# Optimization experiments

Hardware: AMD Instinct MI355X
Metric: run time of the kernel (lower is better)

The kernel has to match this reference:

```python
import jax, jax.numpy as jnp
import numpy as np

B, M, F_N, D, GS, L = 32, 512, 64, 128, 4, 8  # batch, max atoms, in feats, int_d, graph channels, layers


def setup_inputs() -> dict:
    key = jax.random.key(0)
    ks = jax.random.split(key, 8)
    G = jax.random.uniform(ks[0], (B, GS, M, M), dtype=jnp.float32)      # dense multi-channel adjacency
    x = jax.random.normal(ks[1], (B, M, F_N), dtype=jnp.float32)          # per-atom features
    W0 = jax.random.normal(ks[2], (GS, F_N, D), dtype=jnp.float32) * 0.05 # per-channel Linear, layer 0
    b0 = jax.random.normal(ks[3], (GS, D), dtype=jnp.float32) * 0.05
    Wl = jax.random.normal(ks[4], (L - 1, GS, D, D), dtype=jnp.float32) * 0.05
    bl = jax.random.normal(ks[5], (L - 1, GS, D), dtype=jnp.float32) * 0.05
    Wout = jax.random.normal(ks[6], (D, 1), dtype=jnp.float32) * 0.05
    bout = jax.random.normal(ks[7], (1,), dtype=jnp.float32) * 0.05
    return {"G": G, "x": x, "W0": W0, "b0": b0, "Wl": Wl, "bl": bl, "Wout": Wout, "bout": bout}


def _graph_mat_layer(G, h, W, b):
    # per-channel linear: [B,M,C] x [GS,C,P] -> [B,GS,M,P]
    multi = jnp.einsum('bmc,gcp->bgmp', h, W) + b[None, :, None, :]
    # per-sample, per-channel adjacency matmul: [B,GS,M,M] @ [B,GS,M,P]
    xout = jnp.einsum('bgmn,bgnp->bgmp', G, multi)
    # ReLU then goodmax aggregation over graph channels (dim=1)
    return jnp.max(jax.nn.relu(xout), axis=1)  # [B,M,P]


def reference(G, x, W0, b0, Wl, bl, Wout, bout):
    # layer 0: input width F_N != D, so no residual (shape mismatch)
    h = _graph_mat_layer(G, x, W0, b0)
    # layers 1..L-1: resnet skip (shapes match)
    for i in range(L - 1):
        h = _graph_mat_layer(G, h, Wl[i], bl[i]) + h
    # lin_out on [B,M,D] -> [B,M,1]
    return h @ Wout + bout
```

## Files before the change

kernel.cpp:

```cpp
#include <hip/hip_runtime.h>
#include <stdint.h>


#define B_  32
#define M_  512
#define FN_ 64
#define D_  128
#define GS_ 4
#define L_  8

typedef __attribute__((ext_vector_type(8))) short short8;
typedef __attribute__((ext_vector_type(4))) float f32x4;
typedef unsigned short us;

__device__ __forceinline__ us f2bf(float f) {
  union { float f; unsigned int u; } v; v.f = f;
  return (us)((v.u + 0x7FFFu + ((v.u >> 16) & 1u)) >> 16);
}

__device__ __forceinline__ short8 cvt8(float4 a, float4 b) {
  union { unsigned int u[4]; short8 s; } r;
  asm("v_cvt_pk_bf16_f32 %0, %1, %2" : "=v"(r.u[0]) : "v"(a.x), "v"(a.y));
  asm("v_cvt_pk_bf16_f32 %0, %1, %2" : "=v"(r.u[1]) : "v"(a.z), "v"(a.w));
  asm("v_cvt_pk_bf16_f32 %0, %1, %2" : "=v"(r.u[2]) : "v"(b.x), "v"(b.y));
  asm("v_cvt_pk_bf16_f32 %0, %1, %2" : "=v"(r.u[3]) : "v"(b.z), "v"(b.w));
  return r.s;
}

__device__ __forceinline__ void gl16(const void* g, void* l) {
  __builtin_amdgcn_global_load_lds((const __attribute__((address_space(1))) void*)g,
                                   (__attribute__((address_space(3))) void*)l, 16, 0, 0);
}

__global__ void k_convW(const float* __restrict__ W0, const float* __restrict__ Wl,
                        us* __restrict__ W0T, us* __restrict__ WlT) {
  int i = blockIdx.x * blockDim.x + threadIdx.x;
  const int n0 = GS_ * FN_ * D_;
  if (i < n0) {
    int g = i / (FN_ * D_), r = i % (FN_ * D_), c = r / D_, p = r % D_;
    W0T[((size_t)g * D_ + p) * FN_ + c] = f2bf(W0[i]);
  } else {
    int j = i - n0;
    if (j < 7 * GS_ * D_ * D_) {
      int l = j / (GS_ * D_ * D_), r = j % (GS_ * D_ * D_);
      int g = r / (D_ * D_), r2 = r % (D_ * D_), c = r2 / D_, p = r2 % D_;
      WlT[(((size_t)l * GS_ + g) * D_ + p) * D_ + c] = f2bf(Wl[j]);
    }
  }
}

template<int NKA, int CC>
__device__ __forceinline__ void stageA(const us* __restrict__ Wt,
                                       const float* __restrict__ bias,
                                       us* __restrict__ Mw,
                                       const us* hbL, us (*smS)[24576],
                                       int g, int hf, int lr, int kq,
                                       int srow, int scol, int kk, int b, int mt) {
  f32x4 acc[4][4];
#pragma unroll
  for (int i = 0; i < 4; ++i)
#pragma unroll
    for (int j = 0; j < 4; ++j) acc[i][j] = (f32x4){0.f, 0.f, 0.f, 0.f};

#define STGA(bufi, ks) do { \
    us* bb_ = smS[bufi] + g * 6144; \
    _Pragma("unroll") \
    for (int u_ = 0; u_ < 4; ++u_) { \
      const us* sp_ = Wt + (size_t)g * D_ * CC + (size_t)(hf * 64 + u_ * 16 + srow) * CC \
                      + (ks) * 32 + scol; \
      gl16(sp_, bb_ + 2048 + (hf * 4 + u_) * 512); \
    } \
  } while (0)

  STGA(0, 0);
  STGA(1, 1);
  const int cm = (CC == 64) ? 7 : 15;
#pragma unroll
  for (int ks = 0; ks < NKA; ++ks) {
    if (ks < NKA - 1) asm volatile("s_waitcnt vmcnt(4)" ::: "memory");
    else              asm volatile("s_waitcnt vmcnt(0)" ::: "memory");
    __builtin_amdgcn_sched_barrier(0);
    const us* sb = smS[ks % 3] + g * 6144 + 2048;
    short8 af[4], bf[4];
#pragma unroll
    for (int i = 0; i < 4; ++i)
      af[i] = *(const short8*)&hbL[(i * 16 + lr) * 128 + (((ks * 4 + kq) ^ (lr & cm)) << 3)];
#pragma unroll
    for (int j = 0; j < 4; ++j)
      bf[j] = *(const short8*)&sb[(hf * 64 + j * 16 + lr) * 32 + kk];
    if (ks + 2 < NKA) STGA((ks + 2) % 3, ks + 2);
    asm volatile("s_waitcnt lgkmcnt(0)" ::: "memory");
    __builtin_amdgcn_sched_barrier(0);
#pragma unroll
    for (int i = 0; i < 4; ++i)
#pragma unroll
      for (int j = 0; j < 4; ++j)
        acc[i][j] = __builtin_amdgcn_mfma_f32_16x16x32_bf16(af[i], bf[j], acc[i][j], 0, 0, 0);
  }
#undef STGA

#pragma unroll
  for (int j = 0; j < 4; ++j) {
    const int p = hf * 64 + j * 16 + lr;
    const float bv = bias[g * D_ + p];
    us* op = Mw + ((size_t)(b * GS_ + g) * D_ + p) * M_;
#pragma unroll
    for (int i = 0; i < 4; ++i) {
      const int n0 = mt * 64 + i * 16 + kq * 4;
      f32x4 v = acc[i][j];
      ushort4 o;
      o.x = f2bf(v[0] + bv); o.y = f2bf(v[1] + bv);
      o.z = f2bf(v[2] + bv); o.w = f2bf(v[3] + bv);
      *(ushort4*)(op + n0) = o;
    }
  }
}

__launch_bounds__(512, 1)
__global__ void k_pre(const float* __restrict__ x,
                      const us* __restrict__ W0T, const float* __restrict__ b0,
                      us* __restrict__ Mh0) {
  __shared__ __align__(16) us smS[2][24576];
  __shared__ __align__(16) us hbL[8192];

  const int bid = blockIdx.x;
  const int swz = (bid & 7) * 32 + (bid >> 3);
  const int b = swz >> 3, mt = swz & 7;

  const int t = threadIdx.x;
  const int w = t >> 6, g = w >> 1, hf = w & 1;
  const int lane = t & 63, lr = lane & 15, kq = lane >> 4;
  const int srow = lane >> 2;
  const int scol = ((lane & 3) ^ ((lane >> 3) & 3)) * 8;
  const int kk = (kq ^ ((lr >> 1) & 3)) * 8;

  {
    const int row = t >> 3, c8 = t & 7;
    const float* xs = x + ((size_t)b * M_ + mt * 64 + row) * FN_ + c8 * 8;
    float4 v0 = *(const float4*)xs, v1 = *(const float4*)(xs + 4);
    ushort4 o0, o1;
    o0.x = f2bf(v0.x); o0.y = f2bf(v0.y); o0.z = f2bf(v0.z); o0.w = f2bf(v0.w);
    o1.x = f2bf(v1.x); o1.y = f2bf(v1.y); o1.z = f2bf(v1.z); o1.w = f2bf(v1.w);
    us* dp = hbL + row * 128 + ((c8 ^ (row & 7)) << 3);
    *(ushort4*)dp = o0; *(ushort4*)(dp + 4) = o1;
  }
  __syncthreads();

  stageA<FN_ / 32, FN_>(W0T, b0, Mh0, hbL, smS, g, hf, lr, kq, srow, scol, kk, b, mt);
}

__launch_bounds__(512, 1)
__global__ void k_fusedC(const float* __restrict__ G, const us* __restrict__ Min,
                         us* __restrict__ Mout, us* __restrict__ Gh,
                         const us* __restrict__ WT, const float* __restrict__ bias,
                         float* __restrict__ h) {
  __shared__ __align__(16) us smS[3][24576];
  __shared__ __align__(16) us hbL[8192];

  const int bid = blockIdx.x;
  const int swz = (bid & 7) * 32 + (bid >> 3);
  const int b = swz >> 3, mt = swz & 7;

  const int t = threadIdx.x;
  const int w = t >> 6, g = w >> 1, hf = w & 1;
  const int lane = t & 63, lr = lane & 15, kq = lane >> 4;
  const int srow = lane >> 2;
  const int scol = ((lane & 3) ^ ((lane >> 3) & 3)) * 8;
  const int kk = (kq ^ ((lr >> 1) & 3)) * 8;
  const int m_l = t >> 3, pq = t & 7;

  const float* Ag = G + ((size_t)(b * GS_ + g) * M_ + mt * 64) * M_;
  us* Ghp = Gh + ((size_t)(b * GS_ + g) * M_ + mt * 64) * M_;
  const us* BgB = Min + (size_t)(b * GS_ + g) * D_ * M_;

#define STGC(bufi, ks) do { \
    us* bb_ = smS[bufi] + g * 6144; \
    _Pragma("unroll") \
    for (int u_ = 0; u_ < 4; ++u_) { \
      const int ls_ = 4 + hf * 4 + u_; \
      const us* sp_ = BgB + (size_t)((ls_ - 4) * 16 + srow) * M_ + (ks) * 32 + scol; \
      gl16(sp_, bb_ + ls_ * 512 + lane * 8); \
    } \
  } while (0)

#define LDA(AR, ks) do { \
    _Pragma("unroll") \
    for (int i_ = 0; i_ < 4; ++i_) { \
      const float* ap_ = Ag + (size_t)(i_ * 16 + lr) * M_ + (ks) * 32 + kq * 8; \
      AR[2 * i_]     = *(const float4*)ap_; \
      AR[2 * i_ + 1] = *(const float4*)(ap_ + 4); \
    } \
  } while (0)

#define BODY(ks, AR) do { \
    if ((ks) < 15) asm volatile("s_waitcnt vmcnt(12)" ::: "memory"); \
    else           asm volatile("s_waitcnt vmcnt(0)" ::: "memory"); \
    __builtin_amdgcn_sched_barrier(0); \
    short8 af[4], bf[4]; \
    _Pragma("unroll") \
    for (int i_ = 0; i_ < 4; ++i_) af[i_] = cvt8(AR[2 * i_], AR[2 * i_ + 1]); \
    if (hf == 0) { \
      _Pragma("unroll") \
      for (int i_ = 0; i_ < 4; ++i_) \
        *(short8*)(Ghp + (size_t)(i_ * 16 + lr) * M_ + (ks) * 32 + kq * 8) = af[i_]; \
    } \
    { const us* sb_ = smS[(ks) % 3] + g * 6144 + 2048; \
      _Pragma("unroll") \
      for (int j_ = 0; j_ < 4; ++j_) \
        bf[j_] = *(const short8*)&sb_[(hf * 64 + j_ * 16 + lr) * 32 + kk]; } \
    if ((ks) + 2 < 16) { LDA(AR, (ks) + 2); STGC(((ks) + 2) % 3, (ks) + 2); } \
    asm volatile("s_waitcnt lgkmcnt(0)" ::: "memory"); \
    __builtin_amdgcn_sched_barrier(0); \
    _Pragma("unroll") \
    for (int i_ = 0; i_ < 4; ++i_) \
      _Pragma("unroll") \
      for (int j_ = 0; j_ < 4; ++j_) \
        acc[i_][j_] = __builtin_amdgcn_mfma_f32_16x16x32_bf16(af[i_], bf[j_], acc[i_][j_], 0, 0, 0); \
  } while (0)

  f32x4 acc[4][4];
#pragma unroll
  for (int i = 0; i < 4; ++i)
#pragma unroll
    for (int j = 0; j < 4; ++j) acc[i][j] = (f32x4){0.f, 0.f, 0.f, 0.f};

  float4 aA[8], aB[8];
  LDA(aA, 0); STGC(0, 0);
  LDA(aB, 1); STGC(1, 1);

#pragma unroll
  for (int kp = 0; kp < 8; ++kp) {
    BODY(2 * kp, aA);
    BODY(2 * kp + 1, aB);
  }
#undef BODY
#undef LDA
#undef STGC

  __syncthreads();

  {
    float* red = (float*)smS + (size_t)g * 8192;
#pragma unroll
    for (int i = 0; i < 4; ++i)
#pragma unroll
      for (int j = 0; j < 4; ++j) {
        const int col = hf * 64 + j * 16 + lr;
        const int ch = col >> 2, cw = col & 3;
#pragma unroll
        for (int cc = 0; cc < 4; ++cc) {
          const int row = i * 16 + kq * 4 + cc;
          red[row * 128 + ((ch ^ (row & 7)) << 2) + cw] = fmaxf(acc[i][j][cc], 0.f);
        }
      }
  }
  __syncthreads();

  f32x4 hreg[4];
  {
    const float* red = (const float*)smS;
#pragma unroll
    for (int k = 0; k < 4; ++k) {
      const int ch = pq * 4 + k;
      const float* rp = red + (size_t)m_l * 128 + ((ch ^ (m_l & 7)) << 2);
      f32x4 v = *(const f32x4*)rp;
#pragma unroll
      for (int gg = 1; gg < 4; ++gg) {
        f32x4 u = *(const f32x4*)(rp + (size_t)gg * 8192);
        v[0] = fmaxf(v[0], u[0]); v[1] = fmaxf(v[1], u[1]);
        v[2] = fmaxf(v[2], u[2]); v[3] = fmaxf(v[3], u[3]);
      }
      hreg[k] = v;
    }
  }
  const size_t ho = ((size_t)b * M_ + mt * 64 + m_l) * D_ + pq * 16;
  float4* hp = (float4*)(h + ho);
#pragma unroll
  for (int k = 0; k < 4; ++k)
    hp[k] = (float4){hreg[k][0], hreg[k][1], hreg[k][2], hreg[k][3]};
  us* d0 = hbL + m_l * 128 + (((2 * pq) ^ (m_l & 15)) << 3);
  us* d1 = hbL + m_l * 128 + (((2 * pq + 1) ^ (m_l & 15)) << 3);
  ushort4 o0, o1, o2, o3;
  o0.x = f2bf(hreg[0][0]); o0.y = f2bf(hreg[0][1]); o0.z = f2bf(hreg[0][2]); o0.w = f2bf(hreg[0][3]);
  o1.x = f2bf(hreg[1][0]); o1.y = f2bf(hreg[1][1]); o1.z = f2bf(hreg[1][2]); o1.w = f2bf(hreg[1][3]);
  o2.x = f2bf(hreg[2][0]); o2.y = f2bf(hreg[2][1]); o2.z = f2bf(hreg[2][2]); o2.w = f2bf(hreg[2][3]);
  o3.x = f2bf(hreg[3][0]); o3.y = f2bf(hreg[3][1]); o3.z = f2bf(hreg[3][2]); o3.w = f2bf(hreg[3][3]);
  *(ushort4*)d0 = o0; *(ushort4*)(d0 + 4) = o1;
  *(ushort4*)d1 = o2; *(ushort4*)(d1 + 4) = o3;
  __syncthreads();

  stageA<D_ / 32, D_>(WT, bias, Mout, hbL, (us (*)[24576])smS, g, hf, lr, kq, srow, scol, kk, b, mt);
}

template<int FIRST, int LAST>
__launch_bounds__(512, 1)
__global__ void k_fused(const us* __restrict__ Gh, const us* __restrict__ Min,
                        us* __restrict__ Mout,
                        const us* __restrict__ WT, const float* __restrict__ bias,
                        float* __restrict__ h,
                        const float* __restrict__ Wout, const float* __restrict__ bout,
                        float* __restrict__ out) {
  __shared__ __align__(16) us smS[3][24576];
  __shared__ __align__(16) us hbL[8192];

  const int bid = blockIdx.x;
  const int swz = (bid & 7) * 32 + (bid >> 3);
  const int b = swz >> 3, mt = swz & 7;

  const int t = threadIdx.x;
  const int w = t >> 6, g = w >> 1, hf = w & 1;
  const int lane = t & 63, lr = lane & 15, kq = lane >> 4;
  const int srow = lane >> 2;
  const int scol = ((lane & 3) ^ ((lane >> 3) & 3)) * 8;
  const int kk = (kq ^ ((lr >> 1) & 3)) * 8;
  const int m_l = t >> 3, pq = t & 7;

  const us* AgB = Gh + ((size_t)(b * GS_ + g) * M_ + mt * 64) * M_;
  const us* BgB = Min + (size_t)(b * GS_ + g) * D_ * M_;
  f32x4 acc[4][4];
#pragma unroll
  for (int i = 0; i < 4; ++i)
#pragma unroll
    for (int j = 0; j < 4; ++j) acc[i][j] = (f32x4){0.f, 0.f, 0.f, 0.f};

#define STGB(bufi, ks) do { \
    us* bb_ = smS[bufi] + g * 6144; \
    _Pragma("unroll") \
    for (int u_ = 0; u_ < 6; ++u_) { \
      const int ls_ = hf * 6 + u_; \
      const us* sp_ = (ls_ < 4) \
        ? AgB + (size_t)(ls_ * 16 + srow) * M_ + (ks) * 32 + scol \
        : BgB + (size_t)((ls_ - 4) * 16 + srow) * M_ + (ks) * 32 + scol; \
      gl16(sp_, bb_ + ls_ * 512 + lane * 8); \
    } \
  } while (0)

  STGB(0, 0);
  STGB(1, 1);
#pragma unroll
  for (int ks = 0; ks < 16; ++ks) {
    if (ks < 15) asm volatile("s_waitcnt vmcnt(6)" ::: "memory");
    else         asm volatile("s_waitcnt vmcnt(0)" ::: "memory");
    __builtin_amdgcn_s_barrier();
    __builtin_amdgcn_sched_barrier(0);
    const us* sa = smS[ks % 3] + g * 6144;
    const us* sb = sa + 2048;
    short8 af[4], bf[4];
#pragma unroll
    for (int i = 0; i < 4; ++i)
      af[i] = *(const short8*)&sa[(i * 16 + lr) * 32 + kk];
#pragma unroll
    for (int j = 0; j < 4; ++j)
      bf[j] = *(const short8*)&sb[(hf * 64 + j * 16 + lr) * 32 + kk];
    if (ks + 2 < 16) STGB((ks + 2) % 3, ks + 2);
    asm volatile("s_waitcnt lgkmcnt(0)" ::: "memory");
    __builtin_amdgcn_sched_barrier(0);
#pragma unroll
    for (int i = 0; i < 4; ++i)
#pragma unroll
      for (int j = 0; j < 4; ++j)
        acc[i][j] = __builtin_amdgcn_mfma_f32_16x16x32_bf16(af[i], bf[j], acc[i][j], 0, 0, 0);
  }
#undef STGB

  __builtin_amdgcn_s_barrier();
  __builtin_amdgcn_sched_barrier(0);

  {
    float* red = (float*)smS + (size_t)g * 8192;
#pragma unroll
    for (int i = 0; i < 4; ++i)
#pragma unroll
      for (int j = 0; j < 4; ++j) {
        const int col = hf * 64 + j * 16 + lr;
        const int ch = col >> 2, cw = col & 3;
#pragma unroll
        for (int cc = 0; cc < 4; ++cc) {
          const int row = i * 16 + kq * 4 + cc;
          red[row * 128 + ((ch ^ (row & 7)) << 2) + cw] = fmaxf(acc[i][j][cc], 0.f);
        }
      }
  }
  __builtin_amdgcn_s_barrier();
  __builtin_amdgcn_sched_barrier(0);

  f32x4 hreg[4];
  {
    const float* red = (const float*)smS;
#pragma unroll
    for (int k = 0; k < 4; ++k) {
      const int ch = pq * 4 + k;
      const float* rp = red + (size_t)m_l * 128 + ((ch ^ (m_l & 7)) << 2);
      f32x4 v = *(const f32x4*)rp;
#pragma unroll
      for (int gg = 1; gg < 4; ++gg) {
        f32x4 u = *(const f32x4*)(rp + (size_t)gg * 8192);
        v[0] = fmaxf(v[0], u[0]); v[1] = fmaxf(v[1], u[1]);
        v[2] = fmaxf(v[2], u[2]); v[3] = fmaxf(v[3], u[3]);
      }
      hreg[k] = v;
    }
  }
  const size_t ho = ((size_t)b * M_ + mt * 64 + m_l) * D_ + pq * 16;
  float4* hp = (float4*)(h + ho);
  if (!FIRST) {
#pragma unroll
    for (int k = 0; k < 4; ++k) {
      float4 hv = hp[k];
      hreg[k][0] += hv.x; hreg[k][1] += hv.y; hreg[k][2] += hv.z; hreg[k][3] += hv.w;
    }
  }

  if constexpr (!LAST) {
#pragma unroll
    for (int k = 0; k < 4; ++k)
      hp[k] = (float4){hreg[k][0], hreg[k][1], hreg[k][2], hreg[k][3]};
    us* d0 = hbL + m_l * 128 + (((2 * pq) ^ (m_l & 15)) << 3);
    us* d1 = hbL + m_l * 128 + (((2 * pq + 1) ^ (m_l & 15)) << 3);
    ushort4 o0, o1, o2, o3;
    o0.x = f2bf(hreg[0][0]); o0.y = f2bf(hreg[0][1]); o0.z = f2bf(hreg[0][2]); o0.w = f2bf(hreg[0][3]);
    o1.x = f2bf(hreg[1][0]); o1.y = f2bf(hreg[1][1]); o1.z = f2bf(hreg[1][2]); o1.w = f2bf(hreg[1][3]);
    o2.x = f2bf(hreg[2][0]); o2.y = f2bf(hreg[2][1]); o2.z = f2bf(hreg[2][2]); o2.w = f2bf(hreg[2][3]);
    o3.x = f2bf(hreg[3][0]); o3.y = f2bf(hreg[3][1]); o3.z = f2bf(hreg[3][2]); o3.w = f2bf(hreg[3][3]);
    *(ushort4*)d0 = o0; *(ushort4*)(d0 + 4) = o1;
    *(ushort4*)d1 = o2; *(ushort4*)(d1 + 4) = o3;
    __syncthreads();

    stageA<D_ / 32, D_>(WT, bias, Mout, hbL, smS, g, hf, lr, kq, srow, scol, kk, b, mt);
  } else {
    float s = 0.f;
#pragma unroll
    for (int k = 0; k < 4; ++k) {
      const float4 wv = *(const float4*)(Wout + pq * 16 + k * 4);
      s += hreg[k][0] * wv.x + hreg[k][1] * wv.y + hreg[k][2] * wv.z + hreg[k][3] * wv.w;
    }
    s += __shfl_xor(s, 1);
    s += __shfl_xor(s, 2);
    s += __shfl_xor(s, 4);
    if (pq == 0) out[(size_t)b * M_ + mt * 64 + m_l] = s + bout[0];
  }
}

extern "C" void kernel_launch(void* const* d_in, const int* in_sizes, int n_in,
                              void* d_out, int out_size, void* d_ws, size_t ws_size,
                              hipStream_t stream) {
  const float* G    = (const float*)d_in[0];
  const float* x    = (const float*)d_in[1];
  const float* W0   = (const float*)d_in[2];
  const float* b0   = (const float*)d_in[3];
  const float* Wl   = (const float*)d_in[4];
  const float* bl   = (const float*)d_in[5];
  const float* Wout = (const float*)d_in[6];
  const float* bout = (const float*)d_in[7];

  char* ws = (char*)d_ws;
  us*   Gh  = (us*)(ws);
  us*   Mh0 = (us*)(ws + 67108864);
  us*   Mh1 = (us*)(ws + 83886080);
  float* h  = (float*)(ws + 100663296);
  us*   W0T = (us*)(ws + 109051904);
  us*   WlT = (us*)(ws + 109051904 + 65536);
  float* out = (float*)d_out;

  k_convW<<<1920, 256, 0, stream>>>(W0, Wl, W0T, WlT);
  k_pre<<<256, 512, 0, stream>>>(x, W0T, b0, Mh0);

  k_fusedC<<<256, 512, 0, stream>>>(G, Mh0, Mh1,
      Gh, WlT + (size_t)0 * GS_ * D_ * D_, bl + (size_t)0 * GS_ * D_, h);

  for (int l = 1; l < L_ - 1; ++l) {
    const us* Min = (l & 1) ? Mh1 : Mh0;
    us* Mout      = (l & 1) ? Mh0 : Mh1;
    k_fused<0, 0><<<256, 512, 0, stream>>>(Gh, Min, Mout,
        WlT + (size_t)l * GS_ * D_ * D_, bl + (size_t)l * GS_ * D_,
        h, Wout, bout, out);
  }
  k_fused<0, 1><<<256, 512, 0, stream>>>(Gh, (L_ - 1) & 1 ? Mh1 : Mh0, nullptr,
      nullptr, nullptr, h, Wout, bout, out);
}
```

Before: 274.1 us.

## Stage fp32 adjacency tiles through LDS with double-buffered async loads in first fused layer

The first fused layer kernel previously loaded fp32 G tiles straight into registers and used a triple-buffered LDS ring for only the B operand. It now stages both the fp32 A tile and the bf16 B tile into LDS with async global-to-LDS loads, using a two-stage double buffer and explicit barriers. The bf16 write-back of G is also split across both half-waves instead of being done by one. The intent is to cut register pressure and improve latency hiding for the large fp32 G stream, at the cost of extra LDS traffic and two block barriers per k-step.

```diff
diff --git a/kernel.cpp b/kernel.cpp
--- a/kernel.cpp
+++ b/kernel.cpp
@@ -150,12 +150,12 @@
 }
 
 __launch_bounds__(512, 1)
-__global__ void k_fusedC(const float* __restrict__ G, const us* __restrict__ Min,
-                         us* __restrict__ Mout, us* __restrict__ Gh,
-                         const us* __restrict__ WT, const float* __restrict__ bias,
-                         float* __restrict__ h) {
-  __shared__ __align__(16) us smS[3][24576];
-  __shared__ __align__(16) us hbL[8192];
+__global__ void k_fusedC2(const float* __restrict__ G, const us* __restrict__ Min,
+                          us* __restrict__ Mout, us* __restrict__ Gh,
+                          const us* __restrict__ WT, const float* __restrict__ bias,
+                          float* __restrict__ h) {
+  __shared__ __align__(16) us sm[81920];
+  us* hbL = sm + 73728;
 
   const int bid = blockIdx.x;
   const int swz = (bid & 7) * 32 + (bid >> 3);
@@ -165,82 +165,85 @@
   const int w = t >> 6, g = w >> 1, hf = w & 1;
   const int lane = t & 63, lr = lane & 15, kq = lane >> 4;
   const int srow = lane >> 2;
-  const int scol = ((lane & 3) ^ ((lane >> 3) & 3)) * 8;
+  const int scolB = ((lane & 3) ^ ((lane >> 3) & 3)) * 8;
   const int kk = (kq ^ ((lr >> 1) & 3)) * 8;
+  const int arow = lane >> 3;
+  const int acol = ((lane & 7) ^ (arow & 7)) * 4;
   const int m_l = t >> 3, pq = t & 7;
 
-  const float* Ag = G + ((size_t)(b * GS_ + g) * M_ + mt * 64) * M_;
+  const float* Agf = G + ((size_t)(b * GS_ + g) * M_ + mt * 64) * M_;
   us* Ghp = Gh + ((size_t)(b * GS_ + g) * M_ + mt * 64) * M_;
-  const us* BgB = Min + (size_t)(b * GS_ + g) * D_ * M_;
-
-#define STGC(bufi, ks) do { \
-    us* bb_ = smS[bufi] + g * 6144; \
+  const us* Bg = Min + (size_t)(b * GS_ + g) * D_ * M_;
+
+#define BUF(ks) (((ks) & 1) * 32768 + g * 8192)
+#define STAGE2(ks) do { \
+    us* ab_ = sm + BUF(ks); \
     _Pragma("unroll") \
     for (int u_ = 0; u_ < 4; ++u_) { \
-      const int ls_ = 4 + hf * 4 + u_; \
-      const us* sp_ = BgB + (size_t)((ls_ - 4) * 16 + srow) * M_ + (ks) * 32 + scol; \
-      gl16(sp_, bb_ + ls_ * 512 + lane * 8); \
+      const int s_ = hf * 4 + u_; \
+      gl16(Agf + (size_t)(s_ * 8 + arow) * M_ + (ks) * 32 + acol, \
+           ab_ + s_ * 512 + lane * 8); \
+      gl16(Bg + (size_t)(s_ * 16 + srow) * M_ + (ks) * 32 + scolB, \
+           ab_ + 4096 + s_ * 512 + lane * 8); \
     } \
   } while (0)
 
-#define LDA(AR, ks) do { \
-    _Pragma("unroll") \
-    for (int i_ = 0; i_ < 4; ++i_) { \
-      const float* ap_ = Ag + (size_t)(i_ * 16 + lr) * M_ + (ks) * 32 + kq * 8; \
-      AR[2 * i_]     = *(const float4*)ap_; \
-      AR[2 * i_ + 1] = *(const float4*)(ap_ + 4); \
-    } \
-  } while (0)
-
-#define BODY(ks, AR) do { \
-    if ((ks) < 15) asm volatile("s_waitcnt vmcnt(12)" ::: "memory"); \
-    else           asm volatile("s_waitcnt vmcnt(0)" ::: "memory"); \
-    __builtin_amdgcn_sched_barrier(0); \
-    short8 af[4], bf[4]; \
-    _Pragma("unroll") \
-    for (int i_ = 0; i_ < 4; ++i_) af[i_] = cvt8(AR[2 * i_], AR[2 * i_ + 1]); \
-    if (hf == 0) { \
-      _Pragma("unroll") \
-      for (int i_ = 0; i_ < 4; ++i_) \
-        *(short8*)(Ghp + (size_t)(i_ * 16 + lr) * M_ + (ks) * 32 + kq * 8) = af[i_]; \
-    } \
-    { const us* sb_ = smS[(ks) % 3] + g * 6144 + 2048; \
-      _Pragma("unroll") \
-      for (int j_ = 0; j_ < 4; ++j_) \
-        bf[j_] = *(const short8*)&sb_[(hf * 64 + j_ * 16 + lr) * 32 + kk]; } \
-    if ((ks) + 2 < 16) { LDA(AR, (ks) + 2); STGC(((ks) + 2) % 3, (ks) + 2); } \
-    asm volatile("s_waitcnt lgkmcnt(0)" ::: "memory"); \
-    __builtin_amdgcn_sched_barrier(0); \
-    _Pragma("unroll") \
-    for (int i_ = 0; i_ < 4; ++i_) \
-      _Pragma("unroll") \
-      for (int j_ = 0; j_ < 4; ++j_) \
-        acc[i_][j_] = __builtin_amdgcn_mfma_f32_16x16x32_bf16(af[i_], bf[j_], acc[i_][j_], 0, 0, 0); \
-  } while (0)
-
   f32x4 acc[4][4];
 #pragma unroll
   for (int i = 0; i < 4; ++i)
 #pragma unroll
     for (int j = 0; j < 4; ++j) acc[i][j] = (f32x4){0.f, 0.f, 0.f, 0.f};
 
-  float4 aA[8], aB[8];
-  LDA(aA, 0); STGC(0, 0);
-  LDA(aB, 1); STGC(1, 1);
-
-#pragma unroll
-  for (int kp = 0; kp < 8; ++kp) {
-    BODY(2 * kp, aA);
-    BODY(2 * kp + 1, aB);
-  }
-#undef BODY
-#undef LDA
-#undef STGC
+  STAGE2(0);
+  STAGE2(1);
+
+#pragma unroll
+  for (int ks = 0; ks < 16; ++ks) {
+    if (ks == 0)      asm volatile("s_waitcnt vmcnt(8)" ::: "memory");
+    else if (ks < 15) asm volatile("s_waitcnt vmcnt(10)" ::: "memory");
+    else              asm volatile("s_waitcnt vmcnt(2)" ::: "memory");
+    __builtin_amdgcn_s_barrier();
+    __builtin_amdgcn_sched_barrier(0);
+    const us* ab = sm + BUF(ks);
+    float4 ar[8];
+#pragma unroll
+    for (int i = 0; i < 4; ++i) {
+      const int row = i * 16 + lr;
+#pragma unroll
+      for (int e = 0; e < 2; ++e)
+        ar[2 * i + e] = *(const float4*)&ab[(row * 8 + ((kq * 2 + e) ^ (row & 7))) * 8];
+    }
+    const us* sb = ab + 4096;
+    short8 bf[4];
+#pragma unroll
+    for (int j = 0; j < 4; ++j)
+      bf[j] = *(const short8*)&sb[(hf * 64 + j * 16 + lr) * 32 + kk];
+    asm volatile("s_waitcnt lgkmcnt(0)" ::: "memory");
+    __builtin_amdgcn_sched_barrier(0);
+    short8 af[4];
+#pragma unroll
+    for (int i = 0; i < 4; ++i) af[i] = cvt8(ar[2 * i], ar[2 * i + 1]);
+    __builtin_amdgcn_s_barrier();
+    {
+      const int i0 = hf * 2;
+#pragma unroll
+      for (int ii = 0; ii < 2; ++ii)
+        *(short8*)(Ghp + (size_t)((i0 + ii) * 16 + lr) * M_ + ks * 32 + kq * 8) = af[i0 + ii];
+    }
+    if (ks + 2 < 16) STAGE2(ks + 2);
+#pragma unroll
+    for (int i = 0; i < 4; ++i)
+#pragma unroll
+      for (int j = 0; j < 4; ++j)
+        acc[i][j] = __builtin_amdgcn_mfma_f32_16x16x32_bf16(af[i], bf[j], acc[i][j], 0, 0, 0);
+  }
+#undef STAGE2
+#undef BUF
 
   __syncthreads();
 
   {
-    float* red = (float*)smS + (size_t)g * 8192;
+    float* red = (float*)sm + (size_t)g * 8192;
 #pragma unroll
     for (int i = 0; i < 4; ++i)
 #pragma unroll
@@ -258,7 +261,7 @@
 
   f32x4 hreg[4];
   {
-    const float* red = (const float*)smS;
+    const float* red = (const float*)sm;
 #pragma unroll
     for (int k = 0; k < 4; ++k) {
       const int ch = pq * 4 + k;
@@ -289,7 +292,8 @@
   *(ushort4*)d1 = o2; *(ushort4*)(d1 + 4) = o3;
   __syncthreads();
 
-  stageA<D_ / 32, D_>(WT, bias, Mout, hbL, (us (*)[24576])smS, g, hf, lr, kq, srow, scol, kk, b, mt);
+  stageA<D_ / 32, D_>(WT, bias, Mout, hbL, (us (*)[24576])sm,
+                      g, hf, lr, kq, srow, scolB, kk, b, mt);
 }
 
 template<int FIRST, int LAST>
@@ -465,8 +469,8 @@
   k_convW<<<1920, 256, 0, stream>>>(W0, Wl, W0T, WlT);
   k_pre<<<256, 512, 0, stream>>>(x, W0T, b0, Mh0);
 
-  k_fusedC<<<256, 512, 0, stream>>>(G, Mh0, Mh1,
-      Gh, WlT + (size_t)0 * GS_ * D_ * D_, bl + (size_t)0 * GS_ * D_, h);
+  k_fusedC2<<<256, 512, 0, stream>>>(G, Mh0, Mh1, Gh,
+      WlT + (size_t)0 * GS_ * D_ * D_, bl + (size_t)0 * GS_ * D_, h);
 
   for (int l = 1; l < L_ - 1; ++l) {
     const us* Min = (l & 1) ? Mh1 : Mh0;
```

Measured after the change: 626.3 us. 2.28x slower.
